# Performance work log

Hardware: AMD Instinct MI355X
Metric: run time of the kernel (lower is better)

Reference implementation:

```python
import jax, jax.numpy as jnp
import numpy as np

N_HEADS = 8
EPS = 1e-08


def setup_inputs() -> dict:
    key = jax.random.key(0)
    ks = jax.random.split(key, 6)
    B, T1, T2, C = 8, 2048, 512, 512
    query = jax.random.normal(ks[0], (B, T1, C), dtype=jnp.float32)
    memory = jax.random.normal(ks[1], (B, T2, C), dtype=jnp.float32)
    query_mask = jnp.ones((B, T1), dtype=bool)
    memory_mask = jnp.ones((B, T2), dtype=bool)
    attn_prior = jax.random.uniform(ks[2], (B, T1, T2), dtype=jnp.float32)
    s = 1.0 / np.sqrt(C)
    Wq = jax.random.normal(ks[3], (C, C), dtype=jnp.float32) * s
    Wkv = jax.random.normal(ks[4], (C, 2 * C), dtype=jnp.float32) * s
    Wo = jax.random.normal(ks[5], (C, C), dtype=jnp.float32) * s
    return {"query": query, "query_mask": query_mask, "memory": memory,
            "memory_mask": memory_mask, "attn_prior": attn_prior,
            "Wq": Wq, "Wkv": Wkv, "Wo": Wo}


def reference(query, query_mask, memory, memory_mask, attn_prior, Wq, Wkv, Wo):
    B, T1, C = query.shape
    T2 = memory.shape[1]
    H = N_HEADS
    Dh = C // H
    scale = Dh ** (-0.5)

    # projections (no bias, as in NeMo q_net/kv_net/o_net)
    q = (query @ Wq).reshape(B, T1, H, Dh).transpose(0, 2, 1, 3)       # (B,H,T1,Dh)
    kv = memory @ Wkv                                                    # (B,T2,2C)
    k, v = jnp.split(kv, 2, axis=-1)
    k = k.reshape(B, T2, H, Dh).transpose(0, 2, 1, 3)                    # (B,H,T2,Dh)
    v = v.reshape(B, T2, H, Dh).transpose(0, 2, 1, 3)                    # (B,H,T2,Dh)

    attn_score = jnp.einsum('bhqd,bhkd->bhqk', q, k) * scale            # (B,H,T1,T2)
    mask = memory_mask[:, None, None, :]                                 # (B,1,1,T2)
    attn_score = jnp.where(mask, attn_score, -jnp.inf)

    # log-prior fusion: log_softmax(scores) + log(prior), renormalized via softmax
    log_prior = jnp.log(attn_prior + EPS)[:, None]                       # (B,1,T1,T2)
    attn_score_log = jax.nn.log_softmax(attn_score, axis=-1) + log_prior
    attn_prob = jax.nn.softmax(attn_score_log, axis=-1)
    attn_prob = jnp.where(mask, attn_prob, 0.0)

    y = jnp.einsum('bhqk,bhkd->bqhd', attn_prob, v).reshape(B, T1, C)
    out = y @ Wo
    return out, attn_prob, attn_score
```

## Files before the change

kernel.cpp:

```cpp
#include <hip/hip_runtime.h>
#include <hip/hip_bf16.h>

#define DEV static __device__ __forceinline__

typedef __attribute__((ext_vector_type(8))) short short8;
typedef __attribute__((ext_vector_type(4))) float f32x4;
typedef __attribute__((ext_vector_type(4))) float float4v;
typedef __attribute__((ext_vector_type(4))) unsigned int uint4v;
typedef __attribute__((ext_vector_type(2))) unsigned int uint2v;


DEV unsigned short f2bf(float f) {
  union { float f; unsigned u; } x{f};
  return (unsigned short)((x.u + 0x7fffu + ((x.u >> 16) & 1u)) >> 16);
}

DEV unsigned pack_bf(float lo, float hi) {
  return (unsigned)f2bf(lo) | ((unsigned)f2bf(hi) << 16);
}

DEV float fast_exp2(float x) { return __builtin_amdgcn_exp2f(x); }
DEV float fast_log2(float x) { return __builtin_amdgcn_logf(x); }

DEV f32x4 mfma16(short8 a, short8 b, f32x4 c) {
  return __builtin_amdgcn_mfma_f32_16x16x32_bf16(a, b, c, 0, 0, 0);
}

DEV void gload16(const void* g, void* l) {
  __builtin_amdgcn_global_load_lds(
      (const __attribute__((address_space(1))) unsigned*)g,
      (__attribute__((address_space(3))) unsigned*)l, 16, 0, 0);
}

__global__ __launch_bounds__(256) void transpose_cvt3(
    const float* __restrict__ Wq, const float* __restrict__ Wkv,
    const float* __restrict__ Wo, unsigned short* __restrict__ WqT,
    unsigned short* __restrict__ WkvT, unsigned short* __restrict__ WoT) {
  __shared__ float tile[32][33];
  const int bid = blockIdx.x;
  const float* src;
  unsigned short* dst;
  int Nd, local;
  if (bid < 256) { src = Wq; dst = WqT; Nd = 512; local = bid; }
  else if (bid < 768) { src = Wkv; dst = WkvT; Nd = 1024; local = bid - 256; }
  else { src = Wo; dst = WoT; Nd = 512; local = bid - 768; }
  const int k0 = (local & 15) * 32;
  const int n0 = (local >> 4) * 32;
  const int tx = threadIdx.x & 31, ty = threadIdx.x >> 5;
#pragma unroll
  for (int i = 0; i < 4; ++i)
    tile[ty + i * 8][tx] = src[(size_t)(k0 + ty + i * 8) * Nd + n0 + tx];
  __syncthreads();
#pragma unroll
  for (int i = 0; i < 4; ++i)
    dst[(size_t)(n0 + ty + i * 8) * 512 + k0 + tx] = f2bf(tile[tx][ty + i * 8]);
}

template <int MODE>
__global__ __launch_bounds__(256, 2) void gemm_kernel(
    const void* __restrict__ Aptr, const unsigned short* __restrict__ WT,
    void* __restrict__ out0, void* __restrict__ out1) {
  __shared__ char smemA[16384];
  __shared__ char smemB[16384];
  const int tid = threadIdx.x;
  const int w = tid >> 6, l = tid & 63, c = l & 15, g = l >> 4;
  const int wm = w >> 1, wn = w & 1;

  const int bid = blockIdx.x;
  const int xcd = bid & 7, idx = bid >> 3;
  constexpr int NCB = (MODE == 1) ? 3 : 2;
  constexpr int NRX = (MODE == 1) ? 4 : 16;
  const int row0 = (xcd * NRX + (idx >> NCB)) * 128;
  const int col0 = (idx & ((1 << NCB) - 1)) * 128;

  f32x4 acc[4][4];
#pragma unroll
  for (int m = 0; m < 4; ++m)
#pragma unroll
    for (int n = 0; n < 4; ++n) acc[m][n] = f32x4{0.f, 0.f, 0.f, 0.f};

  for (int kt = 0; kt < 8; ++kt) {
    if (MODE != 2) {
      const int arow = tid >> 1, ahalf = tid & 1;
      const float* asrc =
          (const float*)Aptr + (size_t)(row0 + arow) * 512 + kt * 64 + ahalf * 32;
      float4v av[8];
#pragma unroll
      for (int i = 0; i < 8; ++i) av[i] = *(const float4v*)(asrc + i * 4);
#pragma unroll
      for (int qq = 0; qq < 4; ++qq) {
        uint4v pk;
        pk.x = pack_bf(av[2 * qq][0], av[2 * qq][1]);
        pk.y = pack_bf(av[2 * qq][2], av[2 * qq][3]);
        pk.z = pack_bf(av[2 * qq + 1][0], av[2 * qq + 1][1]);
        pk.w = pack_bf(av[2 * qq + 1][2], av[2 * qq + 1][3]);
        int off = (arow * 128 + ahalf * 64 + qq * 16) ^ ((arow & 7) << 4);
        *(uint4v*)(smemA + off) = pk;
      }
    } else {
#pragma unroll
      for (int cc = 0; cc < 4; ++cc) {
        int o = cc * 4096 + tid * 16;
        int r_ = o >> 7;
        gload16((const char*)Aptr + (size_t)(row0 + r_) * 1024 + kt * 128 +
                    ((o ^ ((r_ & 7) << 4)) & 127),
                smemA + o);
      }
    }
#pragma unroll
    for (int cc = 0; cc < 4; ++cc) {
      int o = cc * 4096 + tid * 16;
      int r_ = o >> 7;
      gload16((const char*)WT + (size_t)(col0 + r_) * 1024 + kt * 128 +
                  ((o ^ ((r_ & 7) << 4)) & 127),
              smemB + o);
    }
    __syncthreads();
#pragma unroll
    for (int s = 0; s < 2; ++s) {
      short8 af[4], bfr[4];
#pragma unroll
      for (int m = 0; m < 4; ++m) {
        int row = wm * 64 + m * 16 + c;
        af[m] = *(const short8*)(smemA +
                                 ((row * 128 + g * 16 + s * 64) ^ ((row & 7) << 4)));
      }
#pragma unroll
      for (int n = 0; n < 4; ++n) {
        int row = wn * 64 + n * 16 + c;
        bfr[n] = *(const short8*)(smemB +
                                  ((row * 128 + g * 16 + s * 64) ^ ((row & 7) << 4)));
      }
      __builtin_amdgcn_s_setprio(1);
#pragma unroll
      for (int m = 0; m < 4; ++m)
#pragma unroll
        for (int n = 0; n < 4; ++n) acc[m][n] = mfma16(af[m], bfr[n], acc[m][n]);
      __builtin_amdgcn_s_setprio(0);
    }
    __syncthreads();
  }

#pragma unroll
  for (int m = 0; m < 4; ++m)
#pragma unroll
    for (int n = 0; n < 4; ++n)
#pragma unroll
      for (int r = 0; r < 4; ++r) {
        float v = acc[m][n][r];
        int grow = row0 + wm * 64 + m * 16 + g * 4 + r;
        int gcol = col0 + wn * 64 + n * 16 + c;
        if (MODE == 0) {
          int bb = grow >> 11, q = grow & 2047, hh = gcol >> 6, d = gcol & 63;
          ((unsigned short*)out0)[(((size_t)bb * 8 + hh) * 2048 + q) * 64 + d] =
              f2bf(v * 0.125f);
        } else if (MODE == 1) {
          int bb = grow >> 9, t2 = grow & 511;
          if (gcol < 512) {
            int hh = gcol >> 6, d = gcol & 63;
            ((unsigned short*)out0)[(((size_t)bb * 8 + hh) * 512 + t2) * 64 + d] =
                f2bf(v);
          } else {
            int hh = (gcol - 512) >> 6, d = gcol & 63;
            ((unsigned short*)out1)[(((size_t)bb * 8 + hh) * 64 + d) * 512 + t2] =
                f2bf(v);
          }
        } else {
          __builtin_nontemporal_store(
              v, (float*)out0 + (size_t)grow * 512 + gcol);
        }
      }
}

__global__ __launch_bounds__(256, 2) void attn_kernel(
    const unsigned short* __restrict__ Qb, const unsigned short* __restrict__ Kb,
    const unsigned short* __restrict__ VTb, const float* __restrict__ prior,
    float* __restrict__ score, float* __restrict__ prob,
    unsigned short* __restrict__ yb) {
  extern __shared__ char smem[];
  char* kl[2] = {smem, smem + 16384};
  char* vl[2] = {smem + 32768, smem + 49152};
  const int tid = threadIdx.x;
  const int w = tid >> 6, l = tid & 63;
  const int c = l & 15, g = l >> 4;
  char* pw = smem + 65536 + w * 4096;

  const int xid = (blockIdx.x & 7) * 256 + (blockIdx.x >> 3);
  const int h = xid & 7, qt = (xid >> 3) & 31, b = xid >> 8;
  const int bh = b * 8 + h;
  const int q0 = qt * 64;

  const char* kbase = (const char*)(Kb + (size_t)bh * 512 * 64);
  const char* vbase = (const char*)(VTb + (size_t)bh * 64 * 512);

  auto stageK = [&](int t, char* dst) {
    const char* src = kbase + (size_t)t * 16384;
#pragma unroll
    for (int i = 0; i < 4; ++i) {
      int o = i * 4096 + tid * 16;
      int row = o >> 7;
      gload16(src + row * 128 + ((o & 127) ^ ((row & 7) << 4)), dst + o);
    }
  };
  auto stageV = [&](int t, char* dst) {
#pragma unroll
    for (int i = 0; i < 4; ++i) {
      int o = i * 4096 + tid * 16;
      int row = o >> 8;
      gload16(vbase + row * 1024 + t * 256 + ((o & 255) ^ ((row & 7) << 4)),
              dst + o);
    }
  };

  stageK(0, kl[0]);
  stageV(0, vl[0]);

  const char* qbase = (const char*)(Qb + ((size_t)bh * 2048 + q0 + w * 16) * 64);
  short8 qf0 = *(const short8*)(qbase + c * 128 + g * 16);
  short8 qf1 = *(const short8*)(qbase + c * 128 + g * 16 + 64);

  const int q = q0 + w * 16 + c;
  float* sb = score + ((size_t)bh * 2048 + q) * 512 + g * 4;
  float* pb = prob + ((size_t)bh * 2048 + q) * 512 + g * 4;
  const float* prb = prior + ((size_t)b * 2048 + q) * 512 + g * 4;

  f32x4 acc[32];
#pragma unroll
  for (int n = 0; n < 32; ++n) acc[n] = f32x4{0.f, 0.f, 0.f, 0.f};
  f32x4 yacc[4];
#pragma unroll
  for (int n = 0; n < 4; ++n) yacc[n] = f32x4{0.f, 0.f, 0.f, 0.f};
  float rsum = 0.f;

  __syncthreads();

#pragma unroll
  for (int t = 0; t < 4; ++t) {
    const int cur = t & 1;
    if (t < 3) {
      stageK(t + 1, kl[cur ^ 1]);
      stageV(t + 1, vl[cur ^ 1]);
    }
    float4v pr[8];
#pragma unroll
    for (int n = 0; n < 8; ++n)
      pr[n] = *(const float4v*)(prb + t * 128 + n * 16);

#pragma unroll
    for (int n = 0; n < 8; ++n) {
      const int a = t * 8 + n;
      const int krow = n * 16 + c;
      const int base = krow * 128 + g * 16;
      short8 kf0 = *(const short8*)(kl[cur] + (base ^ ((krow & 7) << 4)));
      short8 kf1 = *(const short8*)(kl[cur] + ((base + 64) ^ ((krow & 7) << 4)));
      __builtin_amdgcn_s_setprio(1);
      acc[a] = mfma16(kf0, qf0, acc[a]);
      acc[a] = mfma16(kf1, qf1, acc[a]);
      __builtin_amdgcn_s_setprio(0);
    }
#pragma unroll
    for (int n = 0; n < 8; ++n) {
      const int a = t * 8 + n;
      __builtin_nontemporal_store((float4v)acc[a],
                                  (float4v*)(sb + t * 128 + n * 16));
      f32x4 e;
#pragma unroll
      for (int r = 0; r < 4; ++r)
        e[r] = fast_exp2(acc[a][r] * 1.44269504f + fast_log2(pr[n][r] + 1e-8f));
      rsum += (e[0] + e[1]) + (e[2] + e[3]);
      acc[a] = e;
      uint2v u;
      u.x = pack_bf(e[0], e[1]);
      u.y = pack_bf(e[2], e[3]);
      *(uint2v*)(pw + ((c * 256 + n * 32 + g * 8) ^ ((c & 7) << 4))) = u;
    }
#pragma unroll
    for (int s = 0; s < 4; ++s) {
      short8 pf =
          *(const short8*)(pw + ((c * 256 + s * 64 + g * 16) ^ ((c & 7) << 4)));
#pragma unroll
      for (int nt = 0; nt < 4; ++nt) {
        const int vrow = nt * 16 + c;
        short8 vf = *(const short8*)(
            vl[cur] + ((vrow * 256 + s * 64 + g * 16) ^ ((vrow & 7) << 4)));
        __builtin_amdgcn_s_setprio(1);
        yacc[nt] = mfma16(vf, pf, yacc[nt]);
        __builtin_amdgcn_s_setprio(0);
      }
    }
    __syncthreads();
  }

  rsum += __shfl_xor(rsum, 16);
  rsum += __shfl_xor(rsum, 32);
  const float rs = 1.f / rsum;

#pragma unroll
  for (int n = 0; n < 32; ++n) {
    float4v p;
#pragma unroll
    for (int r = 0; r < 4; ++r) p[r] = acc[n][r] * rs;
    __builtin_nontemporal_store(p, (float4v*)(pb + n * 16));
  }

  unsigned short* yb_ =
      yb + ((size_t)b * 2048 + q0 + w * 16 + c) * 512 + h * 64;
#pragma unroll
  for (int nt = 0; nt < 4; ++nt) {
    uint2v u;
    u.x = pack_bf(yacc[nt][0] * rs, yacc[nt][1] * rs);
    u.y = pack_bf(yacc[nt][2] * rs, yacc[nt][3] * rs);
    *(uint2v*)(yb_ + nt * 16 + g * 4) = u;
  }
}


extern "C" void kernel_launch(void* const* d_in, const int* in_sizes, int n_in,
                              void* d_out, int out_size, void* d_ws, size_t ws_size,
                              hipStream_t stream) {
  (void)in_sizes; (void)n_in; (void)out_size;
  const float* query = (const float*)d_in[0];
  const float* memory = (const float*)d_in[2];
  const float* prior = (const float*)d_in[4];
  const float* Wq = (const float*)d_in[5];
  const float* Wkv = (const float*)d_in[6];
  const float* Wo = (const float*)d_in[7];

  float* out = (float*)d_out;
  float* prob = out + (size_t)8 * 2048 * 512;
  float* score = prob + (size_t)64 * 2048 * 512;

  char* ws = (char*)d_ws;
  size_t off = 0;
  unsigned short* WqT = (unsigned short*)(ws + off);  off += (size_t)512 * 512 * 2;
  unsigned short* WkvT = (unsigned short*)(ws + off); off += (size_t)1024 * 512 * 2;
  unsigned short* WoT = (unsigned short*)(ws + off);  off += (size_t)512 * 512 * 2;
  unsigned short* Qb = (unsigned short*)(ws + off);   off += (size_t)64 * 2048 * 64 * 2;
  unsigned short* Kb = (unsigned short*)(ws + off);   off += (size_t)64 * 512 * 64 * 2;
  unsigned short* VT = (unsigned short*)(ws + off);   off += (size_t)64 * 64 * 512 * 2;
  unsigned short* yb = (unsigned short*)(ws + off);   off += (size_t)8 * 2048 * 512 * 2;
  if (ws_size < off) return;

  (void)hipFuncSetAttribute((const void*)attn_kernel,
                            hipFuncAttributeMaxDynamicSharedMemorySize, 81920);

  transpose_cvt3<<<1024, 256, 0, stream>>>(Wq, Wkv, Wo, WqT, WkvT, WoT);
  gemm_kernel<0><<<512, 256, 0, stream>>>(query, WqT, Qb, nullptr);
  gemm_kernel<1><<<256, 256, 0, stream>>>(memory, WkvT, Kb, VT);
  attn_kernel<<<2048, 256, 81920, stream>>>(Qb, Kb, VT, prior, score, prob, yb);
  gemm_kernel<2><<<512, 256, 0, stream>>>(yb, WoT, out, nullptr);
}
```

Before: 228.7 us.

## Drop LDS staging of K/V and run attention with one-wave blocks

The attention kernel now uses 64-thread blocks, each handling 16 query rows, instead of 256-thread blocks with four waves. K and V MFMA operands are read straight from global memory (relying on L1/L2) rather than being double-buffered into LDS with async loads and barriers. This removes the barriers and the large shared-memory footprint, so more blocks can be resident. In exchange, each wave reloads K/V from cache without sharing them across waves, which raises global and L2 traffic, and the reads are no longer prefetched ahead of the MFMAs.

```diff
diff --git a/kernel.cpp b/kernel.cpp
--- a/kernel.cpp
+++ b/kernel.cpp
@@ -172,54 +172,28 @@
       }
 }
 
-__global__ __launch_bounds__(256, 2) void attn_kernel(
+__global__ __launch_bounds__(64, 2) void attn_kernel(
     const unsigned short* __restrict__ Qb, const unsigned short* __restrict__ Kb,
     const unsigned short* __restrict__ VTb, const float* __restrict__ prior,
     float* __restrict__ score, float* __restrict__ prob,
     unsigned short* __restrict__ yb) {
-  extern __shared__ char smem[];
-  char* kl[2] = {smem, smem + 16384};
-  char* vl[2] = {smem + 32768, smem + 49152};
-  const int tid = threadIdx.x;
-  const int w = tid >> 6, l = tid & 63;
+  __shared__ char pw[4096];
+  const int l = threadIdx.x;
   const int c = l & 15, g = l >> 4;
-  char* pw = smem + 65536 + w * 4096;
-
-  const int xid = (blockIdx.x & 7) * 256 + (blockIdx.x >> 3);
-  const int h = xid & 7, qt = (xid >> 3) & 31, b = xid >> 8;
+
+  const int xid = (blockIdx.x & 7) * 1024 + (blockIdx.x >> 3);
+  const int h = xid & 7, qt = (xid >> 3) & 127, b = xid >> 10;
   const int bh = b * 8 + h;
-  const int q0 = qt * 64;
+  const int q0 = qt * 16;
 
   const char* kbase = (const char*)(Kb + (size_t)bh * 512 * 64);
   const char* vbase = (const char*)(VTb + (size_t)bh * 64 * 512);
 
-  auto stageK = [&](int t, char* dst) {
-    const char* src = kbase + (size_t)t * 16384;
-#pragma unroll
-    for (int i = 0; i < 4; ++i) {
-      int o = i * 4096 + tid * 16;
-      int row = o >> 7;
-      gload16(src + row * 128 + ((o & 127) ^ ((row & 7) << 4)), dst + o);
-    }
-  };
-  auto stageV = [&](int t, char* dst) {
-#pragma unroll
-    for (int i = 0; i < 4; ++i) {
-      int o = i * 4096 + tid * 16;
-      int row = o >> 8;
-      gload16(vbase + row * 1024 + t * 256 + ((o & 255) ^ ((row & 7) << 4)),
-              dst + o);
-    }
-  };
-
-  stageK(0, kl[0]);
-  stageV(0, vl[0]);
-
-  const char* qbase = (const char*)(Qb + ((size_t)bh * 2048 + q0 + w * 16) * 64);
+  const char* qbase = (const char*)(Qb + ((size_t)bh * 2048 + q0) * 64);
   short8 qf0 = *(const short8*)(qbase + c * 128 + g * 16);
   short8 qf1 = *(const short8*)(qbase + c * 128 + g * 16 + 64);
 
-  const int q = q0 + w * 16 + c;
+  const int q = q0 + c;
   float* sb = score + ((size_t)bh * 2048 + q) * 512 + g * 4;
   float* pb = prob + ((size_t)bh * 2048 + q) * 512 + g * 4;
   const float* prb = prior + ((size_t)b * 2048 + q) * 512 + g * 4;
@@ -232,15 +206,8 @@
   for (int n = 0; n < 4; ++n) yacc[n] = f32x4{0.f, 0.f, 0.f, 0.f};
   float rsum = 0.f;
 
-  __syncthreads();
-
 #pragma unroll
   for (int t = 0; t < 4; ++t) {
-    const int cur = t & 1;
-    if (t < 3) {
-      stageK(t + 1, kl[cur ^ 1]);
-      stageV(t + 1, vl[cur ^ 1]);
-    }
     float4v pr[8];
 #pragma unroll
     for (int n = 0; n < 8; ++n)
@@ -249,10 +216,9 @@
 #pragma unroll
     for (int n = 0; n < 8; ++n) {
       const int a = t * 8 + n;
-      const int krow = n * 16 + c;
-      const int base = krow * 128 + g * 16;
-      short8 kf0 = *(const short8*)(kl[cur] + (base ^ ((krow & 7) << 4)));
-      short8 kf1 = *(const short8*)(kl[cur] + ((base + 64) ^ ((krow & 7) << 4)));
+      const char* kr = kbase + (size_t)(t * 128 + n * 16 + c) * 128 + g * 16;
+      short8 kf0 = *(const short8*)(kr);
+      short8 kf1 = *(const short8*)(kr + 64);
       __builtin_amdgcn_s_setprio(1);
       acc[a] = mfma16(kf0, qf0, acc[a]);
       acc[a] = mfma16(kf1, qf1, acc[a]);
@@ -280,15 +246,14 @@
           *(const short8*)(pw + ((c * 256 + s * 64 + g * 16) ^ ((c & 7) << 4)));
 #pragma unroll
       for (int nt = 0; nt < 4; ++nt) {
-        const int vrow = nt * 16 + c;
-        short8 vf = *(const short8*)(
-            vl[cur] + ((vrow * 256 + s * 64 + g * 16) ^ ((vrow & 7) << 4)));
+        const char* vr =
+            vbase + (size_t)(nt * 16 + c) * 1024 + t * 256 + s * 64 + g * 16;
+        short8 vf = *(const short8*)(vr);
         __builtin_amdgcn_s_setprio(1);
         yacc[nt] = mfma16(vf, pf, yacc[nt]);
         __builtin_amdgcn_s_setprio(0);
       }
     }
-    __syncthreads();
   }
 
   rsum += __shfl_xor(rsum, 16);
@@ -303,8 +268,7 @@
     __builtin_nontemporal_store(p, (float4v*)(pb + n * 16));
   }
 
-  unsigned short* yb_ =
-      yb + ((size_t)b * 2048 + q0 + w * 16 + c) * 512 + h * 64;
+  unsigned short* yb_ = yb + ((size_t)b * 2048 + q0 + c) * 512 + h * 64;
 #pragma unroll
   for (int nt = 0; nt < 4; ++nt) {
     uint2v u;
@@ -341,12 +305,9 @@
   unsigned short* yb = (unsigned short*)(ws + off);   off += (size_t)8 * 2048 * 512 * 2;
   if (ws_size < off) return;
 
-  (void)hipFuncSetAttribute((const void*)attn_kernel,
-                            hipFuncAttributeMaxDynamicSharedMemorySize, 81920);
-
   transpose_cvt3<<<1024, 256, 0, stream>>>(Wq, Wkv, Wo, WqT, WkvT, WoT);
   gemm_kernel<0><<<512, 256, 0, stream>>>(query, WqT, Qb, nullptr);
   gemm_kernel<1><<<256, 256, 0, stream>>>(memory, WkvT, Kb, VT);
-  attn_kernel<<<2048, 256, 81920, stream>>>(Qb, Kb, VT, prior, score, prob, yb);
+  attn_kernel<<<8192, 64, 0, stream>>>(Qb, Kb, VT, prior, score, prob, yb);
   gemm_kernel<2><<<512, 256, 0, stream>>>(yb, WoT, out, nullptr);
 }
```

Measured after the change: 297.2 us. 29.9% more time.
